# Kernel tuning notes

Measured on AMD Instinct MI355X. Metric: run time of the kernel, lower is better.

## Reference

```python
import jax, jax.numpy as jnp
import numpy as np

N_LOC = 20000
N_EXP = 200000
H = 64
E = 1500000
L = 400000


def setup_inputs() -> dict:
    key = jax.random.key(0)
    ks = jax.random.split(key, 24)
    f = jnp.float32
    w = lambda k, shp: jax.random.normal(k, shp, dtype=f) * 0.1
    # edges: ('location','of','experts'): src in [0,N_LOC), dst in [0,N_EXP)
    src = jax.random.randint(ks[0], (E,), 0, N_LOC)
    dst = jax.random.randint(ks[1], (E,), 0, N_EXP)
    edge_of = jnp.stack([src, dst])          # location -> experts
    edge_rev = jnp.stack([dst, src])         # experts -> location (ToUndirected)
    row = jax.random.randint(ks[2], (L,), 0, N_LOC)
    col = jax.random.randint(ks[3], (L,), 0, N_EXP)
    edge_label_index = jnp.stack([row, col])
    return dict(
        emb_loc=w(ks[4], (N_LOC, H)), emb_exp=w(ks[5], (N_EXP, H)),
        W1l_of=w(ks[6], (H, H)), b1_of=jnp.zeros((H,), f), W1r_of=w(ks[7], (H, H)),
        W1l_rev=w(ks[8], (H, H)), b1_rev=jnp.zeros((H,), f), W1r_rev=w(ks[9], (H, H)),
        W2l_of=w(ks[10], (H, H)), b2_of=jnp.zeros((H,), f), W2r_of=w(ks[11], (H, H)),
        W2l_rev=w(ks[12], (H, H)), b2_rev=jnp.zeros((H,), f), W2r_rev=w(ks[13], (H, H)),
        dW1=w(ks[14], (2 * H, H)), db1=jnp.zeros((H,), f),
        dW2=w(ks[15], (H, 1)), db2=jnp.zeros((1,), f),
        edge_of=edge_of, edge_rev=edge_rev, edge_label_index=edge_label_index,
    )


def _sage(x_src, x_dst, edge, Wl, b, Wr, n_dst):
    # PyG SAGEConv: lin_l(mean of neighbor msgs) + lin_r(x_dst); bias only in lin_l
    s, d = edge[0], edge[1]
    msg = x_src[s]                                   # [E, H] gather
    summed = jax.ops.segment_sum(msg, d, num_segments=n_dst)
    cnt = jax.ops.segment_sum(jnp.ones((edge.shape[1],), x_src.dtype), d, num_segments=n_dst)
    agg = summed / jnp.maximum(cnt, 1.0)[:, None]
    return agg @ Wl + b + x_dst @ Wr


def reference(emb_loc, emb_exp,
              W1l_of, b1_of, W1r_of, W1l_rev, b1_rev, W1r_rev,
              W2l_of, b2_of, W2r_of, W2l_rev, b2_rev, W2r_rev,
              dW1, db1, dW2, db2,
              edge_of, edge_rev, edge_label_index):
    # layer 1 (to_hetero: one conv per edge type; each dst type has one incoming type)
    z_exp = jax.nn.relu(_sage(emb_loc, emb_exp, edge_of, W1l_of, b1_of, W1r_of, N_EXP))
    z_loc = jax.nn.relu(_sage(emb_exp, emb_loc, edge_rev, W1l_rev, b1_rev, W1r_rev, N_LOC))
    # layer 2 (no relu)
    z_exp2 = _sage(z_loc, z_exp, edge_of, W2l_of, b2_of, W2r_of, N_EXP)
    z_loc2 = _sage(z_exp, z_loc, edge_rev, W2l_rev, b2_rev, W2r_rev, N_LOC)
    # EdgeDecoder: gather-concat-MLP
    row, col = edge_label_index[0], edge_label_index[1]
    z = jnp.concatenate([z_loc2[row], z_exp2[col]], axis=-1)  # [L, 2H]
    h = jax.nn.relu(z @ dW1 + db1)
    out = (h @ dW2 + db2).reshape(-1)
    return out
```

## Files before the change

### kernel.cpp

```cpp
#include <hip/hip_runtime.h>

#define H 64
#define NE 1500000
#define NLOC 20000
#define NEXP 200000
#define NL 400000
#define PAD_E 32
#define PAD_L 128

#define EB 896
#define NBE 224
#define LB 112
#define NBL 179
#define BIN_CHUNK 2048
#define NBIN ((NE + BIN_CHUNK - 1) / BIN_CHUNK)
#define EBSLOT 28
#define LBSLOT 32
#define ECAP 8192
#define LCAP 10240
#define FCAP 4096

#define WS_NEED 90546112ULL

typedef int vint4 __attribute__((ext_vector_type(4)));
typedef _Float16 f16x8 __attribute__((ext_vector_type(8)));
typedef _Float16 f16x4 __attribute__((ext_vector_type(4)));
typedef float f32x4 __attribute__((ext_vector_type(4)));
typedef unsigned int u32;
typedef unsigned short u16;
typedef unsigned long long u64;

__device__ __forceinline__ float bcastf(float v, int k) {
  return __int_as_float(__builtin_amdgcn_readlane(__float_as_int(v), k));
}
__device__ __forceinline__ int bcasti(int v, int k) {
  return __builtin_amdgcn_readlane(v, k);
}
__device__ __forceinline__ int sel4(int g, int n0, int n1, int n2, int n3) {
  return (g & 2) ? ((g & 1) ? n3 : n2) : ((g & 1) ? n1 : n0);
}

__global__ __launch_bounds__(256) void bin_kernel(
    const int* __restrict__ src, const int* __restrict__ dst,
    u32* __restrict__ expQ, u32* __restrict__ locQ,
    int* __restrict__ qcnt, int* __restrict__ flbk_cnt,
    u64* __restrict__ flbkQ)
{
  __shared__ u32 eb[NBE * EBSLOT];
  __shared__ u32 lb[NBL * LBSLOT];
  __shared__ int ec[NBE], lc[NBL], ebase[NBE], lbase[NBL];

  const int tid = threadIdx.x;
  for (int i = tid; i < NBE; i += 256) ec[i] = 0;
  for (int i = tid; i < NBL; i += 256) lc[i] = 0;
  __syncthreads();

  const long base = (long)blockIdx.x * BIN_CHUNK + tid * 8;
  if (base < NE) {
    vint4 s0 = __builtin_nontemporal_load((const vint4*)(src + base));
    vint4 s1 = __builtin_nontemporal_load((const vint4*)(src + base + 4));
    vint4 d0 = __builtin_nontemporal_load((const vint4*)(dst + base));
    vint4 d1 = __builtin_nontemporal_load((const vint4*)(dst + base + 4));
    int ss[8] = {s0.x, s0.y, s0.z, s0.w, s1.x, s1.y, s1.z, s1.w};
    int dd[8] = {d0.x, d0.y, d0.z, d0.w, d1.x, d1.y, d1.z, d1.w};
#pragma unroll
    for (int k = 0; k < 8; k++) {
      const u32 d = (u32)dd[k], s = (u32)ss[k];
      {
        const u32 b = d / (u32)EB;
        const int pos = atomicAdd(&ec[b], 1);
        if (pos < EBSLOT) {
          eb[b * EBSLOT + pos] = ((d - b * EB) << 16) | s;
        } else {
          int fi = atomicAdd(flbk_cnt, 1);
          if (fi < FCAP) flbkQ[fi] = ((u64)d << 32) | (u64)s;
        }
      }
      {
        const u32 b = s / (u32)LB;
        const int pos = atomicAdd(&lc[b], 1);
        if (pos < LBSLOT) {
          lb[b * LBSLOT + pos] = ((s - b * LB) << 18) | d;
        } else {
          int fi = atomicAdd(flbk_cnt, 1);
          if (fi < FCAP) flbkQ[fi] = (1ULL << 63) | ((u64)s << 32) | (u64)d;
        }
      }
    }
  }
  __syncthreads();

  for (int i = tid; i < NBE; i += 256) {
    const int c = min(ec[i], EBSLOT);
    ebase[i] = c ? atomicAdd(&qcnt[i], c) : 0;
  }
  for (int i = tid; i < NBL; i += 256) {
    const int c = min(lc[i], LBSLOT);
    lbase[i] = c ? atomicAdd(&qcnt[NBE + i], c) : 0;
  }
  __syncthreads();

  const int wid = tid >> 6, ln = tid & 63;
  for (int b = wid; b < NBE; b += 4) {
    const int c = min(ec[b], EBSLOT);
    if (ln < c) {
      const int idx = ebase[b] + ln;
      const u32 r = eb[b * EBSLOT + ln];
      if (idx < ECAP) {
        expQ[(long)b * ECAP + idx] = r;
      } else {
        int fi = atomicAdd(flbk_cnt, 1);
        if (fi < FCAP)
          flbkQ[fi] = ((u64)(b * EB + (r >> 16)) << 32) | (u64)(r & 0xFFFF);
      }
    }
  }
  for (int b = wid; b < NBL; b += 4) {
    const int c = min(lc[b], LBSLOT);
    if (ln < c) {
      const int idx = lbase[b] + ln;
      const u32 r = lb[b * LBSLOT + ln];
      if (idx < LCAP) {
        locQ[(long)b * LCAP + idx] = r;
      } else {
        int fi = atomicAdd(flbk_cnt, 1);
        if (fi < FCAP)
          flbkQ[fi] = (1ULL << 63) | ((u64)(b * LB + (r >> 18)) << 32) |
                      (u64)(r & 0x3FFFF);
      }
    }
  }
}

__global__ __launch_bounds__(256) void build_kernel(
    const u32* __restrict__ expQ, const u32* __restrict__ locQ,
    const int* __restrict__ qcnt,
    u16* __restrict__ nbr_exp, int* __restrict__ nbr_loc,
    int* __restrict__ cnt_exp, int* __restrict__ cnt_loc)
{
  __shared__ char ldsraw[60928];
  const int tid = threadIdx.x;
  if (blockIdx.x < NBE) {
    const int b = blockIdx.x;
    u16* rows = (u16*)ldsraw;
    int* cnts = (int*)(ldsraw + 57344);
    for (int i = tid; i < EB; i += 256) cnts[i] = 0;
    __syncthreads();
    const int n = min(qcnt[b], ECAP);
    for (int i = tid; i < n; i += 256) {
      const u32 r = expQ[(long)b * ECAP + i];
      const int nl = (int)(r >> 16);
      const int pos = atomicAdd(&cnts[nl], 1);
      if (pos < PAD_E) rows[nl * PAD_E + pos] = (u16)(r & 0xFFFF);
    }
    __syncthreads();
    const int node0 = b * EB;
    const int nn = min(EB, NEXP - node0);
    u32* grows = (u32*)(nbr_exp + (long)node0 * PAD_E);
    const u32* lrows = (const u32*)rows;
    for (int j = tid; j < nn * (PAD_E / 2); j += 256) grows[j] = lrows[j];
    for (int i = tid; i < nn; i += 256) cnt_exp[node0 + i] = cnts[i];
  } else {
    const int b = blockIdx.x - NBE;
    int* rows = (int*)ldsraw;
    int* cnts = (int*)(ldsraw + 57344);
    for (int i = tid; i < LB; i += 256) cnts[i] = 0;
    __syncthreads();
    const int n = min(qcnt[NBE + b], LCAP);
    for (int i = tid; i < n; i += 256) {
      const u32 r = locQ[(long)b * LCAP + i];
      const int sl = (int)(r >> 18);
      const int pos = atomicAdd(&cnts[sl], 1);
      if (pos < PAD_L) rows[sl * PAD_L + pos] = (int)(r & 0x3FFFF);
    }
    __syncthreads();
    const int node0 = b * LB;
    const int nn = min(LB, NLOC - node0);
    int* grows = nbr_loc + (long)node0 * PAD_L;
    for (int j = tid; j < nn * PAD_L; j += 256) grows[j] = rows[j];
    for (int i = tid; i < nn; i += 256) cnt_loc[node0 + i] = cnts[i];
  }
}

__global__ __launch_bounds__(256) void prep_kernel(
    const float* __restrict__ W2r_of, const float* __restrict__ W2l_of,
    const float* __restrict__ W2l_rev, const float* __restrict__ W2r_rev,
    const float* __restrict__ dW1, const float* __restrict__ b2_of,
    const float* __restrict__ b2_rev,
    float* __restrict__ Wf_q, float* __restrict__ Wf_y2,
    float* __restrict__ Wf_t2, float* __restrict__ Wf_p,
    float* __restrict__ bf_q, float* __restrict__ bf_p,
    const int* __restrict__ flbk_cnt, const u64* __restrict__ flbkQ,
    u16* __restrict__ nbr_exp, int* __restrict__ nbr_loc,
    int* __restrict__ cnt_exp, int* __restrict__ cnt_loc,
    const float* __restrict__ emb_loc, _Float16* __restrict__ Ylh,
    const float* __restrict__ W1l_of,
    const float* __restrict__ W1r_of, const float* __restrict__ W1l_rev,
    const float* __restrict__ W1r_rev,
    _Float16* __restrict__ W1rT16, _Float16* __restrict__ W1lrT16,
    _Float16* __restrict__ WfqT16,
    _Float16* __restrict__ W1rRevH16, _Float16* __restrict__ Wt2H16,
    _Float16* __restrict__ WpH16)
{
  const int lane = threadIdx.x & 63;
  const int w = threadIdx.x >> 6;
  const float* dW1a = dW1;
  const float* dW1b = dW1 + H * H;
  if (blockIdx.x < 4) {
    const float* A; const float* B; float* C;
    _Float16* CT; _Float16* CH;
    switch (blockIdx.x) {
      case 0:  A = W2r_of;  B = dW1b; C = Wf_q;  CT = WfqT16; CH = nullptr; break;
      case 1:  A = W2l_of;  B = dW1b; C = Wf_y2; CT = nullptr; CH = nullptr; break;
      case 2:  A = W2l_rev; B = dW1a; C = Wf_t2; CT = nullptr; CH = Wt2H16; break;
      default: A = W2r_rev; B = dW1a; C = Wf_p;  CT = nullptr; CH = WpH16;  break;
    }
    float b[H];
#pragma unroll
    for (int k = 0; k < H; k++) b[k] = B[k * H + lane];
    for (int r = w * 16; r < w * 16 + 16; r++) {
      const float xv = A[r * H + lane];
      float a0 = 0.f, a1 = 0.f;
#pragma unroll
      for (int k = 0; k < H; k += 2) {
        a0 += bcastf(xv, k)     * b[k];
        a1 += bcastf(xv, k + 1) * b[k + 1];
      }
      const float val = a0 + a1;
      C[r * H + lane] = val;
      if (CT) CT[(long)lane * H + r] = (_Float16)val;
      if (CH) CH[(long)r * H + lane] = (_Float16)val;
    }
  } else if (blockIdx.x == 4) {
    if (w < 2) {
      const float* bv_src = (w == 0) ? b2_of : b2_rev;
      const float* B      = (w == 0) ? dW1b  : dW1a;
      float* o            = (w == 0) ? bf_q  : bf_p;
      float wk[H];
#pragma unroll
      for (int k = 0; k < H; k++) wk[k] = B[k * H + lane];
      const float bv = bv_src[lane];
      float a = 0.f;
#pragma unroll
      for (int k = 0; k < H; k++) a += bcastf(bv, k) * wk[k];
      o[lane] = a;
    }
  } else if (blockIdx.x == 5) {
    const int n = min(*flbk_cnt, FCAP);
    for (int i = threadIdx.x; i < n; i += 256) {
      const u64 rec = flbkQ[i];
      const int node = (int)((rec >> 32) & 0x3FFFF);
      const int val  = (int)(rec & 0x3FFFF);
      if ((rec >> 63) == 0) {
        int pos = atomicAdd(&cnt_exp[node], 1);
        if (pos < PAD_E) nbr_exp[(long)node * PAD_E + pos] = (u16)val;
      } else {
        int pos = atomicAdd(&cnt_loc[node], 1);
        if (pos < PAD_L) nbr_loc[(long)node * PAD_L + pos] = val;
      }
    }
  } else if (blockIdx.x < 8) {
    const float* S = (blockIdx.x == 6) ? W1r_of : W1l_rev;
    _Float16* D    = (blockIdx.x == 6) ? W1rT16 : W1lrT16;
    for (int k = w * 16; k < w * 16 + 16; k++)
      D[(long)lane * H + k] = (_Float16)S[(long)k * H + lane];
  } else if (blockIdx.x == 8) {
    for (int k = w * 16; k < w * 16 + 16; k++)
      W1rRevH16[(long)k * H + lane] = (_Float16)W1r_rev[(long)k * H + lane];
  } else {
    float wreg[H];
#pragma unroll
    for (int k = 0; k < H; k++) wreg[k] = W1l_of[k * H + lane];
    const int gw2 = (blockIdx.x - 9) * 4 + w;
    for (int r = gw2; r < NLOC; r += 5000) {
      const float xv = emb_loc[(long)r * H + lane];
      float a0 = 0.f, a1 = 0.f;
#pragma unroll
      for (int k = 0; k < H; k += 2) {
        a0 += bcastf(xv, k)     * wreg[k];
        a1 += bcastf(xv, k + 1) * wreg[k + 1];
      }
      Ylh[(long)r * H + lane] = (_Float16)(a0 + a1);
    }
  }
}

__global__ __launch_bounds__(256, 4) void dense_linear_kernel(
    const float* __restrict__ x, _Float16* __restrict__ out16,
    const float* __restrict__ W, int n)
{
  const int lane = threadIdx.x & 63;
  const int gw = (blockIdx.x * 256 + threadIdx.x) >> 6;
  const int nw = (gridDim.x * 256) >> 6;
  float w[H];
#pragma unroll
  for (int k = 0; k < H; k++) w[k] = W[k * H + lane];
  for (int i = gw; i < n; i += nw) {
    const float xv = x[i * H + lane];
    float a0 = 0.f, a1 = 0.f;
#pragma unroll
    for (int k = 0; k < H; k += 2) {
      a0 += bcastf(xv, k)     * w[k];
      a1 += bcastf(xv, k + 1) * w[k + 1];
    }
    out16[i * H + lane] = (_Float16)(a0 + a1);
  }
}

__global__ __launch_bounds__(256, 4) void mfma_pass_kernel(
    const u16* __restrict__ nbr, const int* __restrict__ cnt,
    const _Float16* __restrict__ y,
    const float* a32, const _Float16* a16,
    _Float16* out1, const _Float16* __restrict__ W1T,
    const float* __restrict__ bias, int relu,
    _Float16* out2, const _Float16* __restrict__ W2T)
{
  const int w = threadIdx.x >> 6;
  const int lane = threadIdx.x & 63;
  const int q = lane >> 4;
  const int cidx = lane & 15;
  const int rb = blockIdx.x * 16;

  __shared__ float Gs[16 * 68];

  const _Float16* bt1 = W1T + (long)(w * 16 + cidx) * H;
  f16x8 b1lo = *(const f16x8*)(bt1 + q * 8);
  f16x8 b1hi = *(const f16x8*)(bt1 + 32 + q * 8);
  f16x8 b2lo, b2hi;
  if (out2) {
    const _Float16* bt2 = W2T + (long)(w * 16 + cidx) * H;
    b2lo = *(const f16x8*)(bt2 + q * 8);
    b2hi = *(const f16x8*)(bt2 + 32 + q * 8);
  }

  f16x8 a0, a1;
  if (a16) {
    const _Float16* ar = a16 + (long)(rb + cidx) * H;
    a0 = *(const f16x8*)(ar + q * 8);
    a1 = *(const f16x8*)(ar + 32 + q * 8);
  } else {
    const float* ar = a32 + (long)(rb + cidx) * H;
    f32x4 v0 = *(const f32x4*)(ar + q * 8);
    f32x4 v1 = *(const f32x4*)(ar + q * 8 + 4);
    f32x4 v2 = *(const f32x4*)(ar + 32 + q * 8);
    f32x4 v3 = *(const f32x4*)(ar + 32 + q * 8 + 4);
#pragma unroll
    for (int j = 0; j < 4; j++) {
      a0[j] = (_Float16)v0[j];
      a0[j + 4] = (_Float16)v1[j];
      a1[j] = (_Float16)v2[j];
      a1[j + 4] = (_Float16)v3[j];
    }
  }

  if (y) {
    const int i0r = rb + w * 4;
    const int g = lane >> 4;
    const int sub = lane & 15;
    int c4v[4];
#pragma unroll
    for (int rr = 0; rr < 4; rr++) c4v[rr] = cnt[i0r + rr];
    int id4[4];
#pragma unroll
    for (int rr = 0; rr < 4; rr++) {
      const int c = min(c4v[rr], PAD_E);
      id4[rr] = (lane < c) ? (int)nbr[(long)(i0r + rr) * PAD_E + lane] : 0;
    }
#pragma unroll
    for (int rr = 0; rr < 4; rr++) {
      const int cc = min(c4v[rr], PAD_E);
      const int id = id4[rr];
      const int kl = cc - 1;
      float s0 = 0.f, s1 = 0.f, s2 = 0.f, s3 = 0.f;
      for (int k = 0; k < cc; k += 4) {
        const int n0 = bcasti(id, k);
        const int n1 = bcasti(id, min(k + 1, kl));
        const int n2 = bcasti(id, min(k + 2, kl));
        const int n3 = bcasti(id, min(k + 3, kl));
        const int ns = sel4(g, n0, n1, n2, n3);
        const f16x4 v = *(const f16x4*)(y + (long)ns * H + sub * 4);
        const float msk = (k + g < cc) ? 1.0f : 0.0f;
        s0 = fmaf(msk, (float)v[0], s0);
        s1 = fmaf(msk, (float)v[1], s1);
        s2 = fmaf(msk, (float)v[2], s2);
        s3 = fmaf(msk, (float)v[3], s3);
      }
      s0 += __shfl_xor(s0, 16); s0 += __shfl_xor(s0, 32);
      s1 += __shfl_xor(s1, 16); s1 += __shfl_xor(s1, 32);
      s2 += __shfl_xor(s2, 16); s2 += __shfl_xor(s2, 32);
      s3 += __shfl_xor(s3, 16); s3 += __shfl_xor(s3, 32);
      const float inv = 1.0f / fmaxf((float)c4v[rr], 1.0f);
      if (lane < 16) {
        float* gp = &Gs[(w * 4 + rr) * 68 + 4 * lane];
        gp[0] = s0 * inv; gp[1] = s1 * inv;
        gp[2] = s2 * inv; gp[3] = s3 * inv;
      }
    }
  }

  f32x4 acc1 = {0.f, 0.f, 0.f, 0.f};
  acc1 = __builtin_amdgcn_mfma_f32_16x16x32_f16(a0, b1lo, acc1, 0, 0, 0);
  acc1 = __builtin_amdgcn_mfma_f32_16x16x32_f16(a1, b1hi, acc1, 0, 0, 0);
  f32x4 acc2 = {0.f, 0.f, 0.f, 0.f};
  if (out2) {
    acc2 = __builtin_amdgcn_mfma_f32_16x16x32_f16(a0, b2lo, acc2, 0, 0, 0);
    acc2 = __builtin_amdgcn_mfma_f32_16x16x32_f16(a1, b2hi, acc2, 0, 0, 0);
  }

  const float bj = bias ? bias[w * 16 + cidx] : 0.f;
  __syncthreads();
#pragma unroll
  for (int reg = 0; reg < 4; reg++) {
    const int r = q * 4 + reg;
    float v = acc1[reg] + bj;
    if (y) v += Gs[r * 68 + w * 16 + cidx];
    if (relu) v = fmaxf(v, 0.f);
    out1[(long)(rb + r) * H + w * 16 + cidx] = (_Float16)v;
    if (out2)
      out2[(long)(rb + r) * H + w * 16 + cidx] = (_Float16)acc2[reg];
  }
}

__global__ __launch_bounds__(256, 4) void fused_loc_kernel(
    const int* __restrict__ nbr, const int* __restrict__ cnt,
    const _Float16* __restrict__ T1, const _Float16* __restrict__ ZEt,
    const float* __restrict__ x,
    float* __restrict__ z_out, _Float16* __restrict__ ph_out,
    const _Float16* __restrict__ Wr16, const _Float16* __restrict__ Wt216,
    const _Float16* __restrict__ Wp16,
    const float* __restrict__ b1, const float* __restrict__ bfp)
{
  __shared__ _Float16 Wl[3 * 4096];
  const int tid = threadIdx.x;
  for (int j = tid * 8; j < 4096; j += 2048) {
    *(f16x8*)&Wl[j]        = *(const f16x8*)&Wr16[j];
    *(f16x8*)&Wl[4096 + j] = *(const f16x8*)&Wt216[j];
    *(f16x8*)&Wl[8192 + j] = *(const f16x8*)&Wp16[j];
  }
  __syncthreads();

  const int lane = tid & 63;
  const int gw = (blockIdx.x * 256 + tid) >> 6;
  const int nw = (gridDim.x * 256) >> 6;
  const int g = lane >> 4;
  const int sub = lane & 15;
  const float bj = b1[lane];
  const float bp = bfp[lane];
  for (int i = gw; i < NLOC; i += nw) {
    const int c = cnt[i];
    const int cc = min(c, PAD_L);
    const int* nb = nbr + (long)i * PAD_L;
    float t0 = 0.f, t1 = 0.f, t2 = 0.f, t3 = 0.f;
    float u0 = 0.f, u1 = 0.f, u2 = 0.f, u3 = 0.f;
    int e = 0;
    while (e < cc) {
      const int m = min(cc - e, 64);
      const int id = (lane < m) ? nb[e + lane] : 0;
      const int ml = m - 1;
      for (int k = 0; k < m; k += 4) {
        const int n0 = bcasti(id, k);
        const int n1 = bcasti(id, min(k + 1, ml));
        const int n2 = bcasti(id, min(k + 2, ml));
        const int n3 = bcasti(id, min(k + 3, ml));
        const int ns = sel4(g, n0, n1, n2, n3);
        const long ro = (long)ns * H + sub * 4;
        const f16x4 vT = *(const f16x4*)(T1 + ro);
        const f16x4 vZ = *(const f16x4*)(ZEt + ro);
        const float mk = (k + g < m) ? 1.0f : 0.0f;
        t0 = fmaf(mk, (float)vT[0], t0);
        t1 = fmaf(mk, (float)vT[1], t1);
        t2 = fmaf(mk, (float)vT[2], t2);
        t3 = fmaf(mk, (float)vT[3], t3);
        u0 = fmaf(mk, (float)vZ[0], u0);
        u1 = fmaf(mk, (float)vZ[1], u1);
        u2 = fmaf(mk, (float)vZ[2], u2);
        u3 = fmaf(mk, (float)vZ[3], u3);
      }
      e += m;
    }
    t0 += __shfl_xor(t0, 16); t0 += __shfl_xor(t0, 32);
    t1 += __shfl_xor(t1, 16); t1 += __shfl_xor(t1, 32);
    t2 += __shfl_xor(t2, 16); t2 += __shfl_xor(t2, 32);
    t3 += __shfl_xor(t3, 16); t3 += __shfl_xor(t3, 32);
    u0 += __shfl_xor(u0, 16); u0 += __shfl_xor(u0, 32);
    u1 += __shfl_xor(u1, 16); u1 += __shfl_xor(u1, 32);
    u2 += __shfl_xor(u2, 16); u2 += __shfl_xor(u2, 32);
    u3 += __shfl_xor(u3, 16); u3 += __shfl_xor(u3, 32);
    const int srcl = lane >> 2;
    const int r2 = lane & 3;
    const float vt0 = __shfl(t0, srcl), vt1 = __shfl(t1, srcl);
    const float vt2 = __shfl(t2, srcl), vt3 = __shfl(t3, srcl);
    const float vu0 = __shfl(u0, srcl), vu1 = __shfl(u1, srcl);
    const float vu2 = __shfl(u2, srcl), vu3 = __shfl(u3, srcl);
    const float inv = 1.0f / fmaxf((float)c, 1.0f);
    const float g1 = ((r2 & 2) ? ((r2 & 1) ? vt3 : vt2)
                               : ((r2 & 1) ? vt1 : vt0)) * inv;
    const float gz = ((r2 & 2) ? ((r2 & 1) ? vu3 : vu2)
                               : ((r2 & 1) ? vu1 : vu0)) * inv;
    const float xv = x[(long)i * H + lane];
    float a0 = 0.f, a1 = 0.f;
#pragma unroll
    for (int k = 0; k < H; k += 2) {
      a0 = fmaf(bcastf(xv, k),     (float)Wl[k * H + lane], a0);
      a1 = fmaf(bcastf(xv, k + 1), (float)Wl[(k + 1) * H + lane], a1);
    }
    const float z = fmaxf(g1 + bj + a0 + a1, 0.0f);
    z_out[(long)i * H + lane] = z;
    float p0 = 0.f, p1 = 0.f;
#pragma unroll
    for (int k = 0; k < H; k += 2) {
      p0 = fmaf(bcastf(gz, k),     (float)Wl[4096 + k * H + lane], p0);
      p0 = fmaf(bcastf(z, k),      (float)Wl[8192 + k * H + lane], p0);
      p1 = fmaf(bcastf(gz, k + 1), (float)Wl[4096 + (k + 1) * H + lane], p1);
      p1 = fmaf(bcastf(z, k + 1),  (float)Wl[8192 + (k + 1) * H + lane], p1);
    }
    ph_out[(long)i * H + lane] = (_Float16)(p0 + p1 + bp);
  }
}

__global__ __launch_bounds__(256, 4) void edge_kernel(
    const int* __restrict__ row, const int* __restrict__ col,
    const _Float16* __restrict__ P, const _Float16* __restrict__ Q,
    const float* __restrict__ db1, const float* __restrict__ dW2,
    const float* __restrict__ db2, float* __restrict__ out)
{
  const int lane = threadIdx.x & 63;
  const int gw = (blockIdx.x * 256 + threadIdx.x) >> 6;
  const int nw = (gridDim.x * 256) >> 6;
  const int g = lane >> 4;
  const int sub = lane & 15;
  const f32x4 bj4 = *(const f32x4*)(db1 + 4 * sub);
  const f32x4 w24 = *(const f32x4*)(dW2 + 4 * sub);
  const float b2 = db2[0];
  for (int e = gw * 4; e < NL; e += nw * 4) {
    const int r0 = row[e], r1 = row[e + 1], r2i = row[e + 2], r3 = row[e + 3];
    const int c0 = col[e], c1 = col[e + 1], c2i = col[e + 2], c3 = col[e + 3];
    const int rs = sel4(g, r0, r1, r2i, r3);
    const int cs = sel4(g, c0, c1, c2i, c3);
    const f16x4 pv = *(const f16x4*)(P + (long)rs * H + sub * 4);
    const f16x4 qv = *(const f16x4*)(Q + (long)cs * H + sub * 4);
    float h = fmaxf((float)pv[0] + (float)qv[0] + bj4[0], 0.f) * w24[0]
            + fmaxf((float)pv[1] + (float)qv[1] + bj4[1], 0.f) * w24[1]
            + fmaxf((float)pv[2] + (float)qv[2] + bj4[2], 0.f) * w24[2]
            + fmaxf((float)pv[3] + (float)qv[3] + bj4[3], 0.f) * w24[3];
    h += __shfl_xor(h, 1);
    h += __shfl_xor(h, 2);
    h += __shfl_xor(h, 4);
    h += __shfl_xor(h, 8);
    if (sub == 0) out[e + g] = h + b2;
  }
}

extern "C" void kernel_launch(void* const* d_in, const int* in_sizes, int n_in,
                              void* d_out, int out_size, void* d_ws, size_t ws_size,
                              hipStream_t stream) {
  const float* emb_loc = (const float*)d_in[0];
  const float* emb_exp = (const float*)d_in[1];
  const float* W1l_of  = (const float*)d_in[2];
  const float* b1_of   = (const float*)d_in[3];
  const float* W1r_of  = (const float*)d_in[4];
  const float* W1l_rev = (const float*)d_in[5];
  const float* b1_rev  = (const float*)d_in[6];
  const float* W1r_rev = (const float*)d_in[7];
  const float* W2l_of  = (const float*)d_in[8];
  const float* b2_of   = (const float*)d_in[9];
  const float* W2r_of  = (const float*)d_in[10];
  const float* W2l_rev = (const float*)d_in[11];
  const float* b2_rev  = (const float*)d_in[12];
  const float* W2r_rev = (const float*)d_in[13];
  const float* dW1     = (const float*)d_in[14];
  const float* db1     = (const float*)d_in[15];
  const float* dW2     = (const float*)d_in[16];
  const float* db2     = (const float*)d_in[17];
  const int*   edge_of = (const int*)d_in[18];
  const int*   eli     = (const int*)d_in[20];

  const int* src = edge_of;
  const int* dst = edge_of + NE;
  const int* row = eli;
  const int* col = eli + NL;

  if (ws_size < WS_NEED) return;

  char* ws = (char*)d_ws;
  int*            cnt_loc = (int*)(ws);
  int*            cnt_exp = (int*)(ws + 80000);
  int*            nbr_loc = (int*)(ws + 880064);
  unsigned short* nbr_exp = (unsigned short*)(ws + 11120064);
  _Float16*       Ylh     = (_Float16*)(ws + 23920064);
  _Float16*       Y2fh    = (_Float16*)(ws + 26480064);
  float*          z_loc   = (float*)(ws + 29040064);
  _Float16*       PH      = (_Float16*)(ws + 34160064);
  _Float16*       W1rT16  = (_Float16*)(ws + 36720064);
  _Float16*       W1lrT16 = (_Float16*)(ws + 36728256);
  _Float16*       WfqT16  = (_Float16*)(ws + 36736448);
  _Float16*       W1rRevH16 = (_Float16*)(ws + 36752832);
  _Float16*       Wt2H16  = (_Float16*)(ws + 36761024);
  _Float16*       WpH16   = (_Float16*)(ws + 36769216);
  _Float16*       ZE      = (_Float16*)(ws + 39280064);
  _Float16*       TH      = (_Float16*)(ws + 64880064);
  u32*            expQ    = (u32*)(ws + 64880064);
  u32*            locQ    = (u32*)(ws + 72220096);
  int*            qcnt    = (int*)(ws + 79551936);
  int*            flbk    = (int*)(ws + 79553552);
  u64*            flbkQ   = (u64*)(ws + 79554048);
  float*          Wf_q    = (float*)(ws + 90480064);
  float*          Wf_y2   = (float*)(ws + 90496448);
  float*          Wf_t2   = (float*)(ws + 90512832);
  float*          Wf_p    = (float*)(ws + 90529216);
  float*          bf_q    = (float*)(ws + 90545600);
  float*          bf_p    = (float*)(ws + 90545856);
  float*          out     = (float*)d_out;

  (void)hipMemsetAsync(ws + 79551936, 0, 2048, stream);

  bin_kernel<<<NBIN, 256, 0, stream>>>(src, dst, expQ, locQ, qcnt, flbk, flbkQ);
  build_kernel<<<NBE + NBL, 256, 0, stream>>>(expQ, locQ, qcnt,
      nbr_exp, nbr_loc, cnt_exp, cnt_loc);
  prep_kernel<<<1259, 256, 0, stream>>>(W2r_of, W2l_of, W2l_rev, W2r_rev,
                                        dW1, b2_of, b2_rev,
                                        Wf_q, Wf_y2, Wf_t2, Wf_p, bf_q, bf_p,
                                        flbk, flbkQ, nbr_exp, nbr_loc,
                                        cnt_exp, cnt_loc,
                                        emb_loc, Ylh, W1l_of,
                                        W1r_of, W1l_rev, W1r_rev,
                                        W1rT16, W1lrT16, WfqT16,
                                        W1rRevH16, Wt2H16, WpH16);

  mfma_pass_kernel<<<NEXP / 16, 256, 0, stream>>>(nbr_exp, cnt_exp, Ylh,
      emb_exp, (const _Float16*)nullptr, ZE, W1rT16, b1_of, 1, TH, W1lrT16);
  fused_loc_kernel<<<2048, 256, 0, stream>>>(nbr_loc, cnt_loc, TH, ZE,
      emb_loc, z_loc, PH, W1rRevH16, Wt2H16, WpH16, b1_rev, bf_p);
  dense_linear_kernel<<<1280, 256, 0, stream>>>(z_loc, Y2fh, Wf_y2, NLOC);
  mfma_pass_kernel<<<NEXP / 16, 256, 0, stream>>>(nbr_exp, cnt_exp, Y2fh,
      (const float*)nullptr, ZE, ZE, WfqT16, bf_q, 0,
      (_Float16*)nullptr, (const _Float16*)nullptr);
  edge_kernel<<<2048, 256, 0, stream>>>(row, col, PH, ZE,
                                        db1, dW2, db2, out);
}
```

Before: 597.7 us.

## Interleave ZE/TH rows, sort loc neighbor lists, fuse dense_linear into loc kernel

The expert-side outputs ZE and TH are now stored interleaved in one 128-wide row (ZT), so the location aggregation fetches both with a single 16-byte load per neighbor. Each location's neighbor list is bitonic-sorted in the build kernel (padded with a sentinel) to improve gather locality. The separate dense_linear kernel and the fp32 z_loc round trip are folded into the location kernel using a new fp16 Wy2 weight, and that kernel now splits each node's edges across four lane groups with one fixed work assignment per wave. The costs are extra sorting work in the build kernel and wider strided stores in the first mfma pass.

```diff
diff --git a/kernel.cpp b/kernel.cpp
--- a/kernel.cpp
+++ b/kernel.cpp
@@ -38,6 +38,13 @@
 }
 __device__ __forceinline__ int sel4(int g, int n0, int n1, int n2, int n3) {
   return (g & 2) ? ((g & 1) ? n3 : n2) : ((g & 1) ? n1 : n0);
+}
+__device__ __forceinline__ float sel4f(int g, float a, float b, float c, float d) {
+  return (g & 2) ? ((g & 1) ? d : c) : ((g & 1) ? b : a);
+}
+__device__ __forceinline__ float sel8f(int i, float a, float b, float c, float d,
+                                       float e, float f, float g2, float h2) {
+  return (i & 4) ? sel4f(i & 3, e, f, g2, h2) : sel4f(i & 3, a, b, c, d);
 }
 
 __global__ __launch_bounds__(256) void bin_kernel(
@@ -165,6 +172,7 @@
     int* rows = (int*)ldsraw;
     int* cnts = (int*)(ldsraw + 57344);
     for (int i = tid; i < LB; i += 256) cnts[i] = 0;
+    for (int i = tid; i < LB * PAD_L; i += 256) rows[i] = 0x3FFFF;
     __syncthreads();
     const int n = min(qcnt[NBE + b], LCAP);
     for (int i = tid; i < n; i += 256) {
@@ -172,6 +180,29 @@
       const int sl = (int)(r >> 18);
       const int pos = atomicAdd(&cnts[sl], 1);
       if (pos < PAD_L) rows[sl * PAD_L + pos] = (int)(r & 0x3FFFF);
+    }
+    __syncthreads();
+    const int ln = tid & 63, wd = tid >> 6;
+    for (int r = wd; r < LB; r += 4) {
+      int* row = rows + r * PAD_L;
+      int v0 = row[ln], v1 = row[64 + ln];
+      for (int k = 2; k <= 128; k <<= 1) {
+        for (int j = k >> 1; j >= 1; j >>= 1) {
+          if (j == 64) {
+            const int a = min(v0, v1), bmx = max(v0, v1);
+            v0 = a; v1 = bmx;
+          } else {
+            const int p0 = __shfl_xor(v0, j);
+            const int p1 = __shfl_xor(v1, j);
+            const bool up = ((ln & j) == 0);
+            const bool a0 = ((ln & k) == 0);
+            const bool a1 = (((ln + 64) & k) == 0);
+            v0 = (up == a0) ? min(v0, p0) : max(v0, p0);
+            v1 = (up == a1) ? min(v1, p1) : max(v1, p1);
+          }
+        }
+      }
+      row[ln] = v0; row[64 + ln] = v1;
     }
     __syncthreads();
     const int node0 = b * LB;
@@ -200,7 +231,7 @@
     _Float16* __restrict__ W1rT16, _Float16* __restrict__ W1lrT16,
     _Float16* __restrict__ WfqT16,
     _Float16* __restrict__ W1rRevH16, _Float16* __restrict__ Wt2H16,
-    _Float16* __restrict__ WpH16)
+    _Float16* __restrict__ WpH16, _Float16* __restrict__ Wy2H16)
 {
   const int lane = threadIdx.x & 63;
   const int w = threadIdx.x >> 6;
@@ -211,7 +242,7 @@
     _Float16* CT; _Float16* CH;
     switch (blockIdx.x) {
       case 0:  A = W2r_of;  B = dW1b; C = Wf_q;  CT = WfqT16; CH = nullptr; break;
-      case 1:  A = W2l_of;  B = dW1b; C = Wf_y2; CT = nullptr; CH = nullptr; break;
+      case 1:  A = W2l_of;  B = dW1b; C = Wf_y2; CT = nullptr; CH = Wy2H16; break;
       case 2:  A = W2l_rev; B = dW1a; C = Wf_t2; CT = nullptr; CH = Wt2H16; break;
       default: A = W2r_rev; B = dW1a; C = Wf_p;  CT = nullptr; CH = WpH16;  break;
     }
@@ -285,35 +316,13 @@
   }
 }
 
-__global__ __launch_bounds__(256, 4) void dense_linear_kernel(
-    const float* __restrict__ x, _Float16* __restrict__ out16,
-    const float* __restrict__ W, int n)
-{
-  const int lane = threadIdx.x & 63;
-  const int gw = (blockIdx.x * 256 + threadIdx.x) >> 6;
-  const int nw = (gridDim.x * 256) >> 6;
-  float w[H];
-#pragma unroll
-  for (int k = 0; k < H; k++) w[k] = W[k * H + lane];
-  for (int i = gw; i < n; i += nw) {
-    const float xv = x[i * H + lane];
-    float a0 = 0.f, a1 = 0.f;
-#pragma unroll
-    for (int k = 0; k < H; k += 2) {
-      a0 += bcastf(xv, k)     * w[k];
-      a1 += bcastf(xv, k + 1) * w[k + 1];
-    }
-    out16[i * H + lane] = (_Float16)(a0 + a1);
-  }
-}
-
 __global__ __launch_bounds__(256, 4) void mfma_pass_kernel(
     const u16* __restrict__ nbr, const int* __restrict__ cnt,
     const _Float16* __restrict__ y,
-    const float* a32, const _Float16* a16,
-    _Float16* out1, const _Float16* __restrict__ W1T,
+    const float* a32, const _Float16* a16, int sa,
+    _Float16* out1, int s1, const _Float16* __restrict__ W1T,
     const float* __restrict__ bias, int relu,
-    _Float16* out2, const _Float16* __restrict__ W2T)
+    _Float16* out2, int s2, const _Float16* __restrict__ W2T)
 {
   const int w = threadIdx.x >> 6;
   const int lane = threadIdx.x & 63;
@@ -335,7 +344,7 @@
 
   f16x8 a0, a1;
   if (a16) {
-    const _Float16* ar = a16 + (long)(rb + cidx) * H;
+    const _Float16* ar = a16 + (long)(rb + cidx) * sa;
     a0 = *(const f16x8*)(ar + q * 8);
     a1 = *(const f16x8*)(ar + 32 + q * 8);
   } else {
@@ -371,7 +380,7 @@
       const int cc = min(c4v[rr], PAD_E);
       const int id = id4[rr];
       const int kl = cc - 1;
-      float s0 = 0.f, s1 = 0.f, s2 = 0.f, s3 = 0.f;
+      float s0 = 0.f, s1v = 0.f, s2v = 0.f, s3 = 0.f;
       for (int k = 0; k < cc; k += 4) {
         const int n0 = bcasti(id, k);
         const int n1 = bcasti(id, min(k + 1, kl));
@@ -381,19 +390,19 @@
         const f16x4 v = *(const f16x4*)(y + (long)ns * H + sub * 4);
         const float msk = (k + g < cc) ? 1.0f : 0.0f;
         s0 = fmaf(msk, (float)v[0], s0);
-        s1 = fmaf(msk, (float)v[1], s1);
-        s2 = fmaf(msk, (float)v[2], s2);
+        s1v = fmaf(msk, (float)v[1], s1v);
+        s2v = fmaf(msk, (float)v[2], s2v);
         s3 = fmaf(msk, (float)v[3], s3);
       }
       s0 += __shfl_xor(s0, 16); s0 += __shfl_xor(s0, 32);
-      s1 += __shfl_xor(s1, 16); s1 += __shfl_xor(s1, 32);
-      s2 += __shfl_xor(s2, 16); s2 += __shfl_xor(s2, 32);
+      s1v += __shfl_xor(s1v, 16); s1v += __shfl_xor(s1v, 32);
+      s2v += __shfl_xor(s2v, 16); s2v += __shfl_xor(s2v, 32);
       s3 += __shfl_xor(s3, 16); s3 += __shfl_xor(s3, 32);
       const float inv = 1.0f / fmaxf((float)c4v[rr], 1.0f);
       if (lane < 16) {
         float* gp = &Gs[(w * 4 + rr) * 68 + 4 * lane];
-        gp[0] = s0 * inv; gp[1] = s1 * inv;
-        gp[2] = s2 * inv; gp[3] = s3 * inv;
+        gp[0] = s0 * inv; gp[1] = s1v * inv;
+        gp[2] = s2v * inv; gp[3] = s3 * inv;
       }
     }
   }
@@ -415,112 +424,112 @@
     float v = acc1[reg] + bj;
     if (y) v += Gs[r * 68 + w * 16 + cidx];
     if (relu) v = fmaxf(v, 0.f);
-    out1[(long)(rb + r) * H + w * 16 + cidx] = (_Float16)v;
+    out1[(long)(rb + r) * s1 + w * 16 + cidx] = (_Float16)v;
     if (out2)
-      out2[(long)(rb + r) * H + w * 16 + cidx] = (_Float16)acc2[reg];
-  }
-}
-
-__global__ __launch_bounds__(256, 4) void fused_loc_kernel(
+      out2[(long)(rb + r) * s2 + w * 16 + cidx] = (_Float16)acc2[reg];
+  }
+}
+
+__global__ __launch_bounds__(256, 5) void loc_fused_kernel(
     const int* __restrict__ nbr, const int* __restrict__ cnt,
-    const _Float16* __restrict__ T1, const _Float16* __restrict__ ZEt,
-    const float* __restrict__ x,
-    float* __restrict__ z_out, _Float16* __restrict__ ph_out,
-    const _Float16* __restrict__ Wr16, const _Float16* __restrict__ Wt216,
-    const _Float16* __restrict__ Wp16,
+    const _Float16* __restrict__ ZT, const float* __restrict__ x,
+    _Float16* __restrict__ y2_out, _Float16* __restrict__ ph_out,
+    const _Float16* __restrict__ Wr16, const _Float16* __restrict__ Wy216,
+    const _Float16* __restrict__ Wt216, const _Float16* __restrict__ Wp16,
     const float* __restrict__ b1, const float* __restrict__ bfp)
 {
-  __shared__ _Float16 Wl[3 * 4096];
+  __shared__ _Float16 Wl[4 * 4096];
   const int tid = threadIdx.x;
   for (int j = tid * 8; j < 4096; j += 2048) {
-    *(f16x8*)&Wl[j]        = *(const f16x8*)&Wr16[j];
-    *(f16x8*)&Wl[4096 + j] = *(const f16x8*)&Wt216[j];
-    *(f16x8*)&Wl[8192 + j] = *(const f16x8*)&Wp16[j];
+    *(f16x8*)&Wl[j]         = *(const f16x8*)&Wr16[j];
+    *(f16x8*)&Wl[4096 + j]  = *(const f16x8*)&Wy216[j];
+    *(f16x8*)&Wl[8192 + j]  = *(const f16x8*)&Wt216[j];
+    *(f16x8*)&Wl[12288 + j] = *(const f16x8*)&Wp16[j];
   }
   __syncthreads();
 
   const int lane = tid & 63;
   const int gw = (blockIdx.x * 256 + tid) >> 6;
-  const int nw = (gridDim.x * 256) >> 6;
-  const int g = lane >> 4;
-  const int sub = lane & 15;
+  const int g = lane >> 4, sub = lane & 15;
   const float bj = b1[lane];
   const float bp = bfp[lane];
-  for (int i = gw; i < NLOC; i += nw) {
-    const int c = cnt[i];
-    const int cc = min(c, PAD_L);
+
+  for (int ep = 0; ep < 4; ep++) {
+    const int i = gw + ep * 5000;
+    const int cf = cnt[i];
+    const int cc = min(cf, PAD_L);
+    const int qlen = (cc + 3) >> 2;
     const int* nb = nbr + (long)i * PAD_L;
-    float t0 = 0.f, t1 = 0.f, t2 = 0.f, t3 = 0.f;
-    float u0 = 0.f, u1 = 0.f, u2 = 0.f, u3 = 0.f;
-    int e = 0;
-    while (e < cc) {
-      const int m = min(cc - e, 64);
-      const int id = (lane < m) ? nb[e + lane] : 0;
-      const int ml = m - 1;
-      for (int k = 0; k < m; k += 4) {
-        const int n0 = bcasti(id, k);
-        const int n1 = bcasti(id, min(k + 1, ml));
-        const int n2 = bcasti(id, min(k + 2, ml));
-        const int n3 = bcasti(id, min(k + 3, ml));
-        const int ns = sel4(g, n0, n1, n2, n3);
-        const long ro = (long)ns * H + sub * 4;
-        const f16x4 vT = *(const f16x4*)(T1 + ro);
-        const f16x4 vZ = *(const f16x4*)(ZEt + ro);
-        const float mk = (k + g < m) ? 1.0f : 0.0f;
-        t0 = fmaf(mk, (float)vT[0], t0);
-        t1 = fmaf(mk, (float)vT[1], t1);
-        t2 = fmaf(mk, (float)vT[2], t2);
-        t3 = fmaf(mk, (float)vT[3], t3);
-        u0 = fmaf(mk, (float)vZ[0], u0);
-        u1 = fmaf(mk, (float)vZ[1], u1);
-        u2 = fmaf(mk, (float)vZ[2], u2);
-        u3 = fmaf(mk, (float)vZ[3], u3);
-      }
-      e += m;
-    }
-    t0 += __shfl_xor(t0, 16); t0 += __shfl_xor(t0, 32);
-    t1 += __shfl_xor(t1, 16); t1 += __shfl_xor(t1, 32);
-    t2 += __shfl_xor(t2, 16); t2 += __shfl_xor(t2, 32);
-    t3 += __shfl_xor(t3, 16); t3 += __shfl_xor(t3, 32);
-    u0 += __shfl_xor(u0, 16); u0 += __shfl_xor(u0, 32);
-    u1 += __shfl_xor(u1, 16); u1 += __shfl_xor(u1, 32);
-    u2 += __shfl_xor(u2, 16); u2 += __shfl_xor(u2, 32);
-    u3 += __shfl_xor(u3, 16); u3 += __shfl_xor(u3, 32);
-    const int srcl = lane >> 2;
-    const int r2 = lane & 3;
-    const float vt0 = __shfl(t0, srcl), vt1 = __shfl(t1, srcl);
-    const float vt2 = __shfl(t2, srcl), vt3 = __shfl(t3, srcl);
-    const float vu0 = __shfl(u0, srcl), vu1 = __shfl(u1, srcl);
-    const float vu2 = __shfl(u2, srcl), vu3 = __shfl(u3, srcl);
-    const float inv = 1.0f / fmaxf((float)c, 1.0f);
-    const float g1 = ((r2 & 2) ? ((r2 & 1) ? vt3 : vt2)
-                               : ((r2 & 1) ? vt1 : vt0)) * inv;
-    const float gz = ((r2 & 2) ? ((r2 & 1) ? vu3 : vu2)
-                               : ((r2 & 1) ? vu1 : vu0)) * inv;
+    const int k0 = g * qlen;
+    const int idq0 = min(nb[min(k0 + sub, PAD_L - 1)], NEXP - 1);
+    const int idq1 = min(nb[min(k0 + 16 + sub, PAD_L - 1)], NEXP - 1);
+
+    float a0 = 0.f, a1 = 0.f, a2 = 0.f, a3 = 0.f;
+    float a4 = 0.f, a5 = 0.f, a6 = 0.f, a7 = 0.f;
+    for (int t = 0; t < qlen; t++) {
+      const int idv = (t < 16) ? idq0 : idq1;
+      const int e = __shfl(idv, (lane & 48) + (t & 15));
+      const float ms = (k0 + t < cc) ? 1.0f : 0.0f;
+      const f16x8 v = *(const f16x8*)(ZT + (long)e * 128 + sub * 8);
+      a0 = fmaf(ms, (float)v[0], a0);
+      a1 = fmaf(ms, (float)v[1], a1);
+      a2 = fmaf(ms, (float)v[2], a2);
+      a3 = fmaf(ms, (float)v[3], a3);
+      a4 = fmaf(ms, (float)v[4], a4);
+      a5 = fmaf(ms, (float)v[5], a5);
+      a6 = fmaf(ms, (float)v[6], a6);
+      a7 = fmaf(ms, (float)v[7], a7);
+    }
+    a0 += __shfl_xor(a0, 16); a0 += __shfl_xor(a0, 32);
+    a1 += __shfl_xor(a1, 16); a1 += __shfl_xor(a1, 32);
+    a2 += __shfl_xor(a2, 16); a2 += __shfl_xor(a2, 32);
+    a3 += __shfl_xor(a3, 16); a3 += __shfl_xor(a3, 32);
+    a4 += __shfl_xor(a4, 16); a4 += __shfl_xor(a4, 32);
+    a5 += __shfl_xor(a5, 16); a5 += __shfl_xor(a5, 32);
+    a6 += __shfl_xor(a6, 16); a6 += __shfl_xor(a6, 32);
+    a7 += __shfl_xor(a7, 16); a7 += __shfl_xor(a7, 32);
+    const int zsrc = lane >> 3;
+    const int tsrc = 8 + (lane >> 3);
+    const float z0 = __shfl(a0, zsrc), z1 = __shfl(a1, zsrc);
+    const float z2 = __shfl(a2, zsrc), z3 = __shfl(a3, zsrc);
+    const float z4 = __shfl(a4, zsrc), z5 = __shfl(a5, zsrc);
+    const float z6 = __shfl(a6, zsrc), z7 = __shfl(a7, zsrc);
+    const float t0 = __shfl(a0, tsrc), t1 = __shfl(a1, tsrc);
+    const float t2 = __shfl(a2, tsrc), t3 = __shfl(a3, tsrc);
+    const float t4 = __shfl(a4, tsrc), t5 = __shfl(a5, tsrc);
+    const float t6 = __shfl(a6, tsrc), t7 = __shfl(a7, tsrc);
+    const int r3 = lane & 7;
+    const float inv = 1.0f / fmaxf((float)cf, 1.0f);
+    const float gz = sel8f(r3, z0, z1, z2, z3, z4, z5, z6, z7) * inv;
+    const float g1 = sel8f(r3, t0, t1, t2, t3, t4, t5, t6, t7) * inv;
     const float xv = x[(long)i * H + lane];
-    float a0 = 0.f, a1 = 0.f;
+    float s0 = 0.f, s1 = 0.f;
 #pragma unroll
     for (int k = 0; k < H; k += 2) {
-      a0 = fmaf(bcastf(xv, k),     (float)Wl[k * H + lane], a0);
-      a1 = fmaf(bcastf(xv, k + 1), (float)Wl[(k + 1) * H + lane], a1);
-    }
-    const float z = fmaxf(g1 + bj + a0 + a1, 0.0f);
-    z_out[(long)i * H + lane] = z;
-    float p0 = 0.f, p1 = 0.f;
+      s0 = fmaf(bcastf(xv, k),     (float)Wl[k * H + lane], s0);
+      s1 = fmaf(bcastf(xv, k + 1), (float)Wl[(k + 1) * H + lane], s1);
+    }
+    const float z = fmaxf(g1 + bj + s0 + s1, 0.0f);
+    float y0 = 0.f, y1 = 0.f, p0 = 0.f, p1 = 0.f;
 #pragma unroll
     for (int k = 0; k < H; k += 2) {
-      p0 = fmaf(bcastf(gz, k),     (float)Wl[4096 + k * H + lane], p0);
-      p0 = fmaf(bcastf(z, k),      (float)Wl[8192 + k * H + lane], p0);
-      p1 = fmaf(bcastf(gz, k + 1), (float)Wl[4096 + (k + 1) * H + lane], p1);
-      p1 = fmaf(bcastf(z, k + 1),  (float)Wl[8192 + (k + 1) * H + lane], p1);
-    }
+      const float zk = bcastf(z, k),  zk1 = bcastf(z, k + 1);
+      const float gk = bcastf(gz, k), gk1 = bcastf(gz, k + 1);
+      y0 = fmaf(zk,  (float)Wl[4096 + k * H + lane], y0);
+      y1 = fmaf(zk1, (float)Wl[4096 + (k + 1) * H + lane], y1);
+      p0 = fmaf(gk,  (float)Wl[8192 + k * H + lane], p0);
+      p0 = fmaf(zk,  (float)Wl[12288 + k * H + lane], p0);
+      p1 = fmaf(gk1, (float)Wl[8192 + (k + 1) * H + lane], p1);
+      p1 = fmaf(zk1, (float)Wl[12288 + (k + 1) * H + lane], p1);
+    }
+    y2_out[(long)i * H + lane] = (_Float16)(y0 + y1);
     ph_out[(long)i * H + lane] = (_Float16)(p0 + p1 + bp);
   }
 }
 
 __global__ __launch_bounds__(256, 4) void edge_kernel(
     const int* __restrict__ row, const int* __restrict__ col,
-    const _Float16* __restrict__ P, const _Float16* __restrict__ Q,
+    const _Float16* __restrict__ P, const _Float16* __restrict__ Q, int qs,
     const float* __restrict__ db1, const float* __restrict__ dW2,
     const float* __restrict__ db2, float* __restrict__ out)
 {
@@ -538,7 +547,7 @@
     const int rs = sel4(g, r0, r1, r2i, r3);
     const int cs = sel4(g, c0, c1, c2i, c3);
     const f16x4 pv = *(const f16x4*)(P + (long)rs * H + sub * 4);
-    const f16x4 qv = *(const f16x4*)(Q + (long)cs * H + sub * 4);
+    const f16x4 qv = *(const f16x4*)(Q + (long)cs * qs + sub * 4);
     float h = fmaxf((float)pv[0] + (float)qv[0] + bj4[0], 0.f) * w24[0]
             + fmaxf((float)pv[1] + (float)qv[1] + bj4[1], 0.f) * w24[1]
             + fmaxf((float)pv[2] + (float)qv[2] + bj4[2], 0.f) * w24[2]
@@ -589,7 +598,6 @@
   unsigned short* nbr_exp = (unsigned short*)(ws + 11120064);
   _Float16*       Ylh     = (_Float16*)(ws + 23920064);
   _Float16*       Y2fh    = (_Float16*)(ws + 26480064);
-  float*          z_loc   = (float*)(ws + 29040064);
   _Float16*       PH      = (_Float16*)(ws + 34160064);
   _Float16*       W1rT16  = (_Float16*)(ws + 36720064);
   _Float16*       W1lrT16 = (_Float16*)(ws + 36728256);
@@ -597,8 +605,8 @@
   _Float16*       W1rRevH16 = (_Float16*)(ws + 36752832);
   _Float16*       Wt2H16  = (_Float16*)(ws + 36761024);
   _Float16*       WpH16   = (_Float16*)(ws + 36769216);
-  _Float16*       ZE      = (_Float16*)(ws + 39280064);
-  _Float16*       TH      = (_Float16*)(ws + 64880064);
+  _Float16*       Wy2H16  = (_Float16*)(ws + 36777472);
+  _Float16*       ZT      = (_Float16*)(ws + 39280064);
   u32*            expQ    = (u32*)(ws + 64880064);
   u32*            locQ    = (u32*)(ws + 72220096);
   int*            qcnt    = (int*)(ws + 79551936);
@@ -625,16 +633,16 @@
                                         emb_loc, Ylh, W1l_of,
                                         W1r_of, W1l_rev, W1r_rev,
                                         W1rT16, W1lrT16, WfqT16,
-                                        W1rRevH16, Wt2H16, WpH16);
+                                        W1rRevH16, Wt2H16, WpH16, Wy2H16);
 
   mfma_pass_kernel<<<NEXP / 16, 256, 0, stream>>>(nbr_exp, cnt_exp, Ylh,
-      emb_exp, (const _Float16*)nullptr, ZE, W1rT16, b1_of, 1, TH, W1lrT16);
-  fused_loc_kernel<<<2048, 256, 0, stream>>>(nbr_loc, cnt_loc, TH, ZE,
-      emb_loc, z_loc, PH, W1rRevH16, Wt2H16, WpH16, b1_rev, bf_p);
-  dense_linear_kernel<<<1280, 256, 0, stream>>>(z_loc, Y2fh, Wf_y2, NLOC);
+      emb_exp, (const _Float16*)nullptr, 0, ZT, 128, W1rT16, b1_of, 1,
+      ZT + 64, 128, W1lrT16);
+  loc_fused_kernel<<<1250, 256, 0, stream>>>(nbr_loc, cnt_loc, ZT,
+      emb_loc, Y2fh, PH, W1rRevH16, Wy2H16, Wt2H16, WpH16, b1_rev, bf_p);
   mfma_pass_kernel<<<NEXP / 16, 256, 0, stream>>>(nbr_exp, cnt_exp, Y2fh,
-      (const float*)nullptr, ZE, ZE, WfqT16, bf_q, 0,
-      (_Float16*)nullptr, (const _Float16*)nullptr);
-  edge_kernel<<<2048, 256, 0, stream>>>(row, col, PH, ZE,
+      (const float*)nullptr, ZT, 128, ZT, 128, WfqT16, bf_q, 0,
+      (_Float16*)nullptr, 0, (const _Float16*)nullptr);
+  edge_kernel<<<2048, 256, 0, stream>>>(row, col, PH, ZT, 128,
                                         db1, dW2, db2, out);
 }
```

Measured after the change: 0.9998 ms. 1.67x slower.
